# Performance work log

Measured on AMD Instinct MI355X. Metric: run time of the kernel, lower is better.

Reference implementation:

```python
import jax, jax.numpy as jnp
from jax import lax
import numpy as np

NEG = -1e30  # safe log-space -inf for fp32 (avoids inf-inf NaNs)
EPS = 1e-7   # keras.backend.epsilon()


def setup_inputs() -> dict:
    key = jax.random.key(0)
    k1, k2 = jax.random.split(key)
    B, T, C, L = 512, 512, 96, 64
    y_true = jax.random.randint(k1, (B, L), 0, C - 1, dtype=jnp.int64)  # labels in [0, C-2]
    # y_pred mimics softmax output: positive, rows sum to 1
    logits = jax.random.uniform(k2, (B, T, C), dtype=jnp.float32)
    y_pred = logits / jnp.sum(logits, axis=-1, keepdims=True)
    return {"y_true": y_true, "y_pred": y_pred}


def _ctc_batch_cost(y_true, y_pred):
    # Faithful to keras.backend.ctc_batch_cost with full input/label lengths
    # and blank index = num_classes - 1.
    B, T, C = y_pred.shape
    L = y_true.shape[1]
    blank = C - 1
    S = 2 * L + 1  # extended label length: blanks interleaved

    logp = jnp.log(y_pred + EPS)  # [B, T, C]

    # extended label sequence: blank, l0, blank, l1, ..., blank
    ext = jnp.full((B, S), blank, dtype=y_true.dtype).at[:, 1::2].set(y_true)  # [B, S]

    # log-probs of extended labels at every time step: [T, B, S]
    lp = jnp.take_along_axis(
        logp, jnp.broadcast_to(ext[:, None, :], (B, T, S)), axis=2
    ).transpose(1, 0, 2)

    # skip transition (s-2 -> s) allowed iff ext[s] != blank and ext[s] != ext[s-2]
    skip = jnp.concatenate(
        [jnp.zeros((B, 2), dtype=bool),
         (ext[:, 2:] != blank) & (ext[:, 2:] != ext[:, :-2])],
        axis=1,
    )  # [B, S]

    # init: alpha_0(0) = logp(blank), alpha_0(1) = logp(l0)
    alpha0 = jnp.full((B, S), NEG, dtype=logp.dtype)
    alpha0 = alpha0.at[:, 0].set(lp[0, :, 0]).at[:, 1].set(lp[0, :, 1])

    def step(alpha, lp_t):
        s1 = jnp.pad(alpha[:, :-1], ((0, 0), (1, 0)), constant_values=NEG)
        s2 = jnp.pad(alpha[:, :-2], ((0, 0), (2, 0)), constant_values=NEG)
        a = jnp.logaddexp(alpha, s1)
        a = jnp.where(skip, jnp.logaddexp(a, s2), a)
        return a + lp_t, None

    alpha, _ = lax.scan(step, alpha0, lp[1:])
    loss = -jnp.logaddexp(alpha[:, -1], alpha[:, -2])  # [B]
    return loss[:, None]  # [B, 1], matching ctc_batch_cost


def reference(y_true, y_pred):
    return _ctc_batch_cost(y_true, y_pred)
```

## Files before the change

### kernel.cpp

```cpp
#include <hip/hip_runtime.h>
#include <math.h>


constexpr int Bv = 512;
constexpr int Tv = 512;
constexpr int Cv = 96;
constexpr int Lv = 64;
constexpr int BLANK = Cv - 1;
constexpr float EPSf = 1e-7f;

constexpr int ROWS = 32;
constexpr int NCH  = Tv / ROWS;
constexpr int CF   = ROWS * Cv;
constexpr int RS   = 100;
constexpr int LBUF = ROWS * RS;

__device__ __forceinline__ float dpp_shr1(float x) {
    return __int_as_float(
        __builtin_amdgcn_update_dpp(0, __float_as_int(x), 0x138, 0xf, 0xf, true));
}
template <int C>
__device__ __forceinline__ float dppmax(float m) {
    return fmaxf(m, __int_as_float(
        __builtin_amdgcn_update_dpp(0, __float_as_int(m), C, 0xf, 0xf, true)));
}

__global__ void __launch_bounds__(64) ctc_fwd(const int* __restrict__ y_true,
                                              const float* __restrict__ y_pred,
                                              float* __restrict__ out) {
    __shared__ float lds[2 * LBUF];

    const int b = blockIdx.x;
    const int l = threadIdx.x;
    const float* __restrict__ yp = y_pred + (size_t)b * (Tv * Cv);

    const int lab   = y_true[b * Lv + l];
    const int labm1 = __shfl_up(lab, 1);
    const bool skip = (l > 0) && (lab != labm1);

#define WA(i) ((((i)*64 + l) / 24) * 400 + (((i)*64 + l) % 24) * 16)
    const int wa0 = WA(0),  wa1 = WA(1),  wa2 = WA(2),  wa3 = WA(3);
    const int wa4 = WA(4),  wa5 = WA(5),  wa6 = WA(6),  wa7 = WA(7);
    const int wa8 = WA(8),  wa9 = WA(9), wa10 = WA(10), wa11 = WA(11);
#undef WA

    float4 G0, G1, G2, G3, G4, G5, G6, G7, G8, G9, G10, G11;
#define GLOAD(g) do { const float* gp_ = (g) + l * 4;                        \
    G0 = *(const float4*)(gp_ +    0); G1 = *(const float4*)(gp_ +  256);    \
    G2 = *(const float4*)(gp_ +  512); G3 = *(const float4*)(gp_ +  768);    \
    G4 = *(const float4*)(gp_ + 1024); G5 = *(const float4*)(gp_ + 1280);    \
    G6 = *(const float4*)(gp_ + 1536); G7 = *(const float4*)(gp_ + 1792);    \
    G8 = *(const float4*)(gp_ + 2048); G9 = *(const float4*)(gp_ + 2304);    \
    G10= *(const float4*)(gp_ + 2560); G11= *(const float4*)(gp_ + 2816); } while (0)
#define SWRITE(bufn) do { char* p_ = (char*)(bufn);                          \
    *(float4*)(p_ + wa0) = G0;  *(float4*)(p_ + wa1) = G1;                   \
    *(float4*)(p_ + wa2) = G2;  *(float4*)(p_ + wa3) = G3;                   \
    *(float4*)(p_ + wa4) = G4;  *(float4*)(p_ + wa5) = G5;                   \
    *(float4*)(p_ + wa6) = G6;  *(float4*)(p_ + wa7) = G7;                   \
    *(float4*)(p_ + wa8) = G8;  *(float4*)(p_ + wa9) = G9;                   \
    *(float4*)(p_ + wa10)= G10; *(float4*)(p_ + wa11)= G11; } while (0)

    float AB0,AB1,AB2,AB3,AB4,AB5,AB6,AB7, AL0,AL1,AL2,AL3,AL4,AL5,AL6,AL7;
    float BB0,BB1,BB2,BB3,BB4,BB5,BB6,BB7, BL0,BL1,BL2,BL3,BL4,BL5,BL6,BL7;
#define LOAD8(P, bb, r0) do { const float* pB_ = (bb) + BLANK;               \
    const float* pL_ = (bb) + lab;                                           \
    P##B0 = pB_[((r0)+0)*RS]; P##L0 = pL_[((r0)+0)*RS];                      \
    P##B1 = pB_[((r0)+1)*RS]; P##L1 = pL_[((r0)+1)*RS];                      \
    P##B2 = pB_[((r0)+2)*RS]; P##L2 = pL_[((r0)+2)*RS];                      \
    P##B3 = pB_[((r0)+3)*RS]; P##L3 = pL_[((r0)+3)*RS];                      \
    P##B4 = pB_[((r0)+4)*RS]; P##L4 = pL_[((r0)+4)*RS];                      \
    P##B5 = pB_[((r0)+5)*RS]; P##L5 = pL_[((r0)+5)*RS];                      \
    P##B6 = pB_[((r0)+6)*RS]; P##L6 = pL_[((r0)+6)*RS];                      \
    P##B7 = pB_[((r0)+7)*RS]; P##L7 = pL_[((r0)+7)*RS]; } while (0)

    float a0, a1, a2;
    int   e_acc = 0;
    float sc_p = 1.0f; int e_p = 0;

    auto step = [&](float PB, float PL) {
        float pb  = PB + EPSf;
        float pl  = PL + EPSf;
        float pls = skip ? pl : 0.0f;
        float a1p = dpp_shr1(a1);
        float t01 = a0 + a1;
        float na1 = fmaf(a1p, pls, t01 * pl);
        float na0 = fmaf(a1p, pb, a0 * pb);
        float na2 = (a2 + a1) * pb;
        a0 = na0; a1 = na1; a2 = na2;
    };
    auto rn_apply = [&]() {
        a0 *= sc_p; a1 *= sc_p; a2 *= sc_p; e_acc += e_p;
    };
    auto rn_compute = [&]() {
        float m = fmaxf(fmaxf(a0, a1), a2);
        m = dppmax<0x111>(m); m = dppmax<0x112>(m); m = dppmax<0x114>(m);
        m = dppmax<0x118>(m); m = dppmax<0x142>(m); m = dppmax<0x143>(m);
        float mw = __int_as_float(__builtin_amdgcn_readlane(__float_as_int(m), 63));
        int e; (void)frexpf(mw, &e);
        sc_p = ldexpf(1.0f, -e); e_p = e;
    };
#define GROUP8(P) do {                                                       \
    step(P##B0, P##L0); step(P##B1, P##L1); step(P##B2, P##L2);              \
    step(P##B3, P##L3); rn_apply();                                          \
    step(P##B4, P##L4); step(P##B5, P##L5); step(P##B6, P##L6);              \
    step(P##B7, P##L7); rn_compute(); } while (0)

    GLOAD(yp);
    SWRITE(lds);
    GLOAD(yp + CF);
    LOAD8(A, lds, 0);
    const bool lane0 = (l == 0);
    a0 = lane0 ? (AB0 + EPSf) : 0.0f;
    a1 = lane0 ? (AL0 + EPSf) : 0.0f;
    a2 = 0.0f;

    for (int c = 0; c < NCH; ++c) {
        float* bufB = lds + (c & 1) * LBUF;
        float* bufN = lds + ((c & 1) ^ 1) * LBUF;

        LOAD8(B, bufB, 8);
        if (c == 0) {
            step(AB1, AL1); step(AB2, AL2); step(AB3, AL3); rn_apply();
            step(AB4, AL4); step(AB5, AL5); step(AB6, AL6); step(AB7, AL7);
            rn_compute();
        } else {
            GROUP8(A);
        }
        LOAD8(A, bufB, 16);
        GROUP8(B);
        LOAD8(B, bufB, 24);
        GROUP8(A);
        if (c < NCH - 1) SWRITE(bufN);
        if (c < NCH - 2) GLOAD(yp + (size_t)(c + 2) * CF);
        if (c < NCH - 1) LOAD8(A, bufN, 0);
        GROUP8(B);
    }

    if (l == 63) {
        float sum = a1 + a2;
        out[b] = -(logf(sum) + (float)e_acc * 0.69314718055994530942f);
    }
#undef GLOAD
#undef SWRITE
#undef LOAD8
#undef GROUP8
}

extern "C" void kernel_launch(void* const* d_in, const int* in_sizes, int n_in,
                              void* d_out, int out_size, void* d_ws, size_t ws_size,
                              hipStream_t stream) {
    const int*   y_true = (const int*)d_in[0];
    const float* y_pred = (const float*)d_in[1];
    float*       out    = (float*)d_out;
    (void)in_sizes; (void)n_in; (void)out_size; (void)d_ws; (void)ws_size;
    ctc_fwd<<<Bv, 64, 0, stream>>>(y_true, y_pred, out);
}
```

Measured before the change: 148.0 us.

## Deepen global prefetch to two chunks and fold epsilon add into LDS write

```diff
diff --git a/kernel.cpp b/kernel.cpp
--- a/kernel.cpp
+++ b/kernel.cpp
@@ -25,9 +25,9 @@
         __builtin_amdgcn_update_dpp(0, __float_as_int(m), C, 0xf, 0xf, true)));
 }
 
-__global__ void __launch_bounds__(64) ctc_fwd(const int* __restrict__ y_true,
-                                              const float* __restrict__ y_pred,
-                                              float* __restrict__ out) {
+__global__ void __launch_bounds__(64, 1) ctc_fwd(const int* __restrict__ y_true,
+                                                 const float* __restrict__ y_pred,
+                                                 float* __restrict__ out) {
     __shared__ float lds[2 * LBUF];
 
     const int b = blockIdx.x;
@@ -45,20 +45,22 @@
 #undef WA
 
     float4 G0, G1, G2, G3, G4, G5, G6, G7, G8, G9, G10, G11;
-#define GLOAD(g) do { const float* gp_ = (g) + l * 4;                        \
-    G0 = *(const float4*)(gp_ +    0); G1 = *(const float4*)(gp_ +  256);    \
-    G2 = *(const float4*)(gp_ +  512); G3 = *(const float4*)(gp_ +  768);    \
-    G4 = *(const float4*)(gp_ + 1024); G5 = *(const float4*)(gp_ + 1280);    \
-    G6 = *(const float4*)(gp_ + 1536); G7 = *(const float4*)(gp_ + 1792);    \
-    G8 = *(const float4*)(gp_ + 2048); G9 = *(const float4*)(gp_ + 2304);    \
-    G10= *(const float4*)(gp_ + 2560); G11= *(const float4*)(gp_ + 2816); } while (0)
-#define SWRITE(bufn) do { char* p_ = (char*)(bufn);                          \
-    *(float4*)(p_ + wa0) = G0;  *(float4*)(p_ + wa1) = G1;                   \
-    *(float4*)(p_ + wa2) = G2;  *(float4*)(p_ + wa3) = G3;                   \
-    *(float4*)(p_ + wa4) = G4;  *(float4*)(p_ + wa5) = G5;                   \
-    *(float4*)(p_ + wa6) = G6;  *(float4*)(p_ + wa7) = G7;                   \
-    *(float4*)(p_ + wa8) = G8;  *(float4*)(p_ + wa9) = G9;                   \
-    *(float4*)(p_ + wa10)= G10; *(float4*)(p_ + wa11)= G11; } while (0)
+    float4 H0, H1, H2, H3, H4, H5, H6, H7, H8, H9, H10, H11;
+#define GLOADS(S, g) do { const float* gp_ = (g) + l * 4;                    \
+    S##0 = *(const float4*)(gp_ +    0); S##1 = *(const float4*)(gp_ +  256);\
+    S##2 = *(const float4*)(gp_ +  512); S##3 = *(const float4*)(gp_ +  768);\
+    S##4 = *(const float4*)(gp_ + 1024); S##5 = *(const float4*)(gp_ + 1280);\
+    S##6 = *(const float4*)(gp_ + 1536); S##7 = *(const float4*)(gp_ + 1792);\
+    S##8 = *(const float4*)(gp_ + 2048); S##9 = *(const float4*)(gp_ + 2304);\
+    S##10= *(const float4*)(gp_ + 2560); S##11= *(const float4*)(gp_ + 2816);} while (0)
+#define E4(v) make_float4((v).x + EPSf, (v).y + EPSf, (v).z + EPSf, (v).w + EPSf)
+#define SWRITES(S, bufn) do { char* p_ = (char*)(bufn);                      \
+    *(float4*)(p_ + wa0) = E4(S##0);  *(float4*)(p_ + wa1) = E4(S##1);       \
+    *(float4*)(p_ + wa2) = E4(S##2);  *(float4*)(p_ + wa3) = E4(S##3);       \
+    *(float4*)(p_ + wa4) = E4(S##4);  *(float4*)(p_ + wa5) = E4(S##5);       \
+    *(float4*)(p_ + wa6) = E4(S##6);  *(float4*)(p_ + wa7) = E4(S##7);       \
+    *(float4*)(p_ + wa8) = E4(S##8);  *(float4*)(p_ + wa9) = E4(S##9);       \
+    *(float4*)(p_ + wa10)= E4(S##10); *(float4*)(p_ + wa11)= E4(S##11); } while (0)
 
     float AB0,AB1,AB2,AB3,AB4,AB5,AB6,AB7, AL0,AL1,AL2,AL3,AL4,AL5,AL6,AL7;
     float BB0,BB1,BB2,BB3,BB4,BB5,BB6,BB7, BL0,BL1,BL2,BL3,BL4,BL5,BL6,BL7;
@@ -77,9 +79,7 @@
     int   e_acc = 0;
     float sc_p = 1.0f; int e_p = 0;
 
-    auto step = [&](float PB, float PL) {
-        float pb  = PB + EPSf;
-        float pl  = PL + EPSf;
+    auto step = [&](float pb, float pl) {
         float pls = skip ? pl : 0.0f;
         float a1p = dpp_shr1(a1);
         float t01 = a0 + a1;
@@ -105,20 +105,21 @@
     step(P##B4, P##L4); step(P##B5, P##L5); step(P##B6, P##L6);              \
     step(P##B7, P##L7); rn_compute(); } while (0)
 
-    GLOAD(yp);
-    SWRITE(lds);
-    GLOAD(yp + CF);
+    GLOADS(G, yp);
+    GLOADS(H, yp + CF);
+    SWRITES(G, lds);
+    GLOADS(G, yp + 2 * CF);
     LOAD8(A, lds, 0);
     const bool lane0 = (l == 0);
-    a0 = lane0 ? (AB0 + EPSf) : 0.0f;
-    a1 = lane0 ? (AL0 + EPSf) : 0.0f;
+    a0 = lane0 ? AB0 : 0.0f;
+    a1 = lane0 ? AL0 : 0.0f;
     a2 = 0.0f;
 
-    for (int c = 0; c < NCH; ++c) {
-        float* bufB = lds + (c & 1) * LBUF;
-        float* bufN = lds + ((c & 1) ^ 1) * LBUF;
+    float* const buf0 = lds;
+    float* const buf1 = lds + LBUF;
 
-        LOAD8(B, bufB, 8);
+    for (int c = 0; c < NCH; c += 2) {
+        LOAD8(B, buf0, 8);
         if (c == 0) {
             step(AB1, AL1); step(AB2, AL2); step(AB3, AL3); rn_apply();
             step(AB4, AL4); step(AB5, AL5); step(AB6, AL6); step(AB7, AL7);
@@ -126,13 +127,24 @@
         } else {
             GROUP8(A);
         }
-        LOAD8(A, bufB, 16);
+        LOAD8(A, buf0, 16);
         GROUP8(B);
-        LOAD8(B, bufB, 24);
+        LOAD8(B, buf0, 24);
         GROUP8(A);
-        if (c < NCH - 1) SWRITE(bufN);
-        if (c < NCH - 2) GLOAD(yp + (size_t)(c + 2) * CF);
-        if (c < NCH - 1) LOAD8(A, bufN, 0);
+        SWRITES(H, buf1);
+        if (c + 3 < NCH) GLOADS(H, yp + (size_t)(c + 3) * CF);
+        LOAD8(A, buf1, 0);
+        GROUP8(B);
+
+        LOAD8(B, buf1, 8);
+        GROUP8(A);
+        LOAD8(A, buf1, 16);
+        GROUP8(B);
+        LOAD8(B, buf1, 24);
+        GROUP8(A);
+        if (c + 1 < NCH - 1) SWRITES(G, buf0);
+        if (c + 4 < NCH) GLOADS(G, yp + (size_t)(c + 4) * CF);
+        if (c + 1 < NCH - 1) LOAD8(A, buf0, 0);
         GROUP8(B);
     }
 
@@ -140,8 +152,9 @@
         float sum = a1 + a2;
         out[b] = -(logf(sum) + (float)e_acc * 0.69314718055994530942f);
     }
-#undef GLOAD
-#undef SWRITE
+#undef GLOADS
+#undef SWRITES
+#undef E4
 #undef LOAD8
 #undef GROUP8
 }
```

Measured after the change: 149.8 us. About the same (+1.2%).
